# Kernel tuning notes

Hardware: AMD Instinct MI355X
Metric: run time of the kernel (lower is better)

Reference implementation:

```python
import jax, jax.numpy as jnp
import numpy as np

N_EMB = 1024
HEAD_SIZE = 128


def setup_inputs() -> dict:
    key = jax.random.key(0)
    k1, k2, k3, k4 = jax.random.split(key, 4)
    B, T = 8, 4096
    x = jax.random.normal(k1, (B, T, N_EMB), dtype=jnp.float32)
    # nn.Linear(n_emb, head_size, bias=False) weights have shape [head_size, n_emb]
    s = 1.0 / np.sqrt(N_EMB)
    Wq = jax.random.uniform(k2, (HEAD_SIZE, N_EMB), jnp.float32, -s, s)
    Wk = jax.random.uniform(k3, (HEAD_SIZE, N_EMB), jnp.float32, -s, s)
    Wv = jax.random.uniform(k4, (HEAD_SIZE, N_EMB), jnp.float32, -s, s)
    return {"x": x, "Wq": Wq, "Wk": Wk, "Wv": Wv}


def reference(x, Wq, Wk, Wv):
    # x: [B, T, C]; W*: [H, C]
    B, T, C = x.shape
    H = Wq.shape[0]
    q = jnp.einsum('btc,hc->bth', x, Wq)
    k = jnp.einsum('btc,hc->bth', x, Wk)
    v = jnp.einsum('btc,hc->bth', x, Wv)
    scale = H ** -0.5
    wei = jnp.einsum('bth,bsh->bts', q, k) * scale  # [B, T, T]
    # causal mask: position t attends to s <= t
    causal = jnp.arange(T)[:, None] >= jnp.arange(T)[None, :]
    wei = jnp.where(causal, wei, -jnp.inf)
    wei = jax.nn.softmax(wei, axis=-1)
    # dropout treated as identity (eval mode)
    out = jnp.einsum('bts,bsh->bth', wei, v)  # [B, T, H]
    return out
```

## Files before the change

kernel.cpp:

```cpp
#include <hip/hip_runtime.h>
#include <hip/hip_bf16.h>

typedef __bf16 bf16_t;
typedef __attribute__((ext_vector_type(8))) __bf16 bf16x8;
typedef __attribute__((ext_vector_type(4))) __bf16 bf16x4;
typedef __attribute__((ext_vector_type(4))) float f32x4;

#define MFMA16(a, b, c) __builtin_amdgcn_mfma_f32_16x16x32_bf16((a), (b), (c), 0, 0, 0)

__device__ __forceinline__ void gload_lds16(const void* g, void* l) {
    __builtin_amdgcn_global_load_lds(
        (const __attribute__((address_space(1))) void*)g,
        (__attribute__((address_space(3))) void*)l, 16, 0, 0);
}

__global__ __launch_bounds__(256, 3) void proj_qkv(
    const float* __restrict__ X,
    const float* __restrict__ W0, const float* __restrict__ W1, const float* __restrict__ W2,
    bf16_t* __restrict__ O0, bf16_t* __restrict__ O1, bf16_t* __restrict__ O2)
{
    __shared__ __align__(16) char As[128 * 128];
    __shared__ __align__(16) char Bs[128 * 128];

    const int tid = threadIdx.x;
    const int wid = tid >> 6;
    const int lane = tid & 63;
    const int l15 = lane & 15, l4 = lane >> 4;
    const int wr = wid >> 1, wc = wid & 1;
    const int m0 = blockIdx.x * 128;

    const float* W = (blockIdx.y == 0) ? W0 : (blockIdx.y == 1 ? W1 : W2);

    const int r0 = tid >> 4;
    const int kq = tid & 15;
    const int swz = ((r0 & 7) << 4);

    f32x4 acc[4][4] = {};
    float4 xr[8];

    #pragma unroll
    for (int i = 0; i < 8; ++i)
        xr[i] = *(const float4*)(X + (size_t)(m0 + r0 + i * 16) * 1024 + kq * 4);

    for (int ks = 0; ks < 16; ++ks) {
        const int kb = ks * 64;
        #pragma unroll
        for (int i = 0; i < 8; ++i) {
            const int r = r0 + i * 16;
            bf16x4 av; av[0] = (bf16_t)xr[i].x; av[1] = (bf16_t)xr[i].y;
            av[2] = (bf16_t)xr[i].z; av[3] = (bf16_t)xr[i].w;
            *(bf16x4*)(As + r * 128 + ((kq * 8) ^ swz)) = av;
        }
        #pragma unroll
        for (int i = 0; i < 8; ++i) {
            const int r = r0 + i * 16;
            float4 wa = *(const float4*)(W + (size_t)r * 1024 + kb + kq * 4);
            bf16x4 wv; wv[0] = (bf16_t)wa.x; wv[1] = (bf16_t)wa.y;
            wv[2] = (bf16_t)wa.z; wv[3] = (bf16_t)wa.w;
            *(bf16x4*)(Bs + r * 128 + ((kq * 8) ^ swz)) = wv;
        }
        __syncthreads();
        if (ks < 15) {
            #pragma unroll
            for (int i = 0; i < 8; ++i)
                xr[i] = *(const float4*)(X + (size_t)(m0 + r0 + i * 16) * 1024 + kb + 64 + kq * 4);
        }
        #pragma unroll
        for (int kk = 0; kk < 64; kk += 32) {
            const int kbyte = 2 * kk + 16 * l4;
            bf16x8 af[4], bfr[4];
            #pragma unroll
            for (int mi = 0; mi < 4; ++mi) {
                int r = wr * 64 + mi * 16 + l15;
                af[mi] = *(const bf16x8*)(As + r * 128 + (kbyte ^ ((r & 7) << 4)));
            }
            #pragma unroll
            for (int ni = 0; ni < 4; ++ni) {
                int r = wc * 64 + ni * 16 + l15;
                bfr[ni] = *(const bf16x8*)(Bs + r * 128 + (kbyte ^ ((r & 7) << 4)));
            }
            #pragma unroll
            for (int mi = 0; mi < 4; ++mi)
                #pragma unroll
                for (int ni = 0; ni < 4; ++ni)
                    acc[mi][ni] = MFMA16(af[mi], bfr[ni], acc[mi][ni]);
        }
        __syncthreads();
    }

    if (blockIdx.y < 2) {
        const float sc = (blockIdx.y == 0) ? 0.12751754816f : 1.0f;
        bf16_t* O = (blockIdx.y == 0) ? O0 : O1;
        #pragma unroll
        for (int mi = 0; mi < 4; ++mi)
            #pragma unroll
            for (int ni = 0; ni < 4; ++ni) {
                int row = m0 + wr * 64 + mi * 16 + l4 * 4;
                int col = wc * 64 + ni * 16 + l15;
                #pragma unroll
                for (int r = 0; r < 4; ++r)
                    O[(size_t)(row + r) * 128 + col] = (bf16_t)(acc[mi][ni][r] * sc);
            }
    } else {
        #pragma unroll
        for (int mi = 0; mi < 4; ++mi)
            #pragma unroll
            for (int ni = 0; ni < 4; ++ni) {
                int row0 = m0 + wr * 64 + mi * 16 + l4 * 4;
                int col = wc * 64 + ni * 16 + l15;
                int bb = row0 >> 12, t0 = row0 & 4095;
                bf16x4 pk;
                #pragma unroll
                for (int r = 0; r < 4; ++r) pk[r] = (bf16_t)acc[mi][ni][r];
                *(bf16x4*)(O2 + ((size_t)bb << 19) + (size_t)col * 4096 + t0) = pk;
            }
    }
}

__global__ __launch_bounds__(256, 2) void attn_fwd(
    const bf16_t* __restrict__ Qb, const bf16_t* __restrict__ Kb,
    const bf16_t* __restrict__ Vtg, float* __restrict__ out, int Bn)
{
    __shared__ __align__(16) char lds[73728];

    const int tid = threadIdx.x, wid = tid >> 6, lane = tid & 63;
    const int l15 = lane & 15, l4 = lane >> 4;
    const int pair = wid >> 1, qh = wid & 1;

    const int blk = blockIdx.x;
    const int b = blk % Bn;
    const int j = blk / Bn;

    const size_t base = (size_t)b * 4096 * 128;
    const size_t baseVT = (size_t)b << 19;

    char* Kbuf = lds + pair * 32768;
    char* Vbuf = Kbuf + 16384;
    char* Pw   = lds + 65536 + wid * 2048;
    const int key = l15 & 7;

    bf16x8 aones;
    #pragma unroll
    for (int e = 0; e < 8; ++e) aones[e] = (bf16_t)1.0f;

    for (int seg = 0; seg < 2; ++seg) {
        const int p = seg ? (127 - j) : j;
        const int q0 = p << 5;
        const int T = (p >> 1) + 1;
        const int smax = (T + 1) >> 1;
        const int qg = q0 + 16 * qh + l15;

        bf16x8 aq[4];
        #pragma unroll
        for (int kf = 0; kf < 4; ++kf)
            aq[kf] = *(const bf16x8*)(Qb + base + (size_t)qg * 128 + 32 * kf + 8 * l4);

        float mx = -1e30f;
        f32x4 ls_acc = (f32x4){0.f, 0.f, 0.f, 0.f};
        f32x4 o[8] = {};

        auto stage = [&](int s) {
            const int lt = 2 * s + pair;
            if (lt >= T) return;
            const int kv0 = lt << 6;
            if (qh == 0) {
                #pragma unroll
                for (int it = 0; it < 16; ++it) {
                    const int row = it * 4 + (lane >> 4);
                    const bf16_t* src = Kb + base + (size_t)(kv0 + row) * 128
                                        + (((lane & 15) ^ (row & 7)) << 3);
                    gload_lds16(src, Kbuf + it * 1024);
                }
            } else {
                #pragma unroll
                for (int it = 0; it < 16; ++it) {
                    const int h = it * 8 + (lane >> 3);
                    const bf16_t* src = Vtg + baseVT + (size_t)h * 4096 + kv0
                                        + (((lane & 7) ^ ((lane >> 3) & 7)) << 3);
                    gload_lds16(src, Vbuf + it * 1024);
                }
            }
        };

        __syncthreads();
        stage(0);
        __syncthreads();

        for (int s = 0; s < smax; ++s) {
            const int lt = 2 * s + pair;
            if (lt < T) {
                const int kv0 = lt << 6;

                f32x4 sa[4];
                #pragma unroll
                for (int ni = 0; ni < 4; ++ni) sa[ni] = (f32x4){0.f, 0.f, 0.f, 0.f};
                __builtin_amdgcn_s_setprio(1);
                #pragma unroll
                for (int kf = 0; kf < 4; ++kf)
                    #pragma unroll
                    for (int ni = 0; ni < 4; ++ni) {
                        bf16x8 ak = *(const bf16x8*)(Kbuf + (16 * ni + l15) * 256
                                                     + (((4 * kf + l4) ^ key) << 4));
                        sa[ni] = MFMA16(ak, aq[kf], sa[ni]);
                    }
                __builtin_amdgcn_s_setprio(0);

                if (lt == T - 1) {
                    #pragma unroll
                    for (int ni = 0; ni < 4; ++ni)
                        #pragma unroll
                        for (int r = 0; r < 4; ++r)
                            if (kv0 + 16 * ni + 4 * l4 + r > qg) sa[ni][r] = -1e30f;
                }

                float tm = -1e30f;
                #pragma unroll
                for (int ni = 0; ni < 4; ++ni)
                    tm = fmaxf(tm, fmaxf(fmaxf(sa[ni][0], sa[ni][1]),
                                         fmaxf(sa[ni][2], sa[ni][3])));
                if (__any(tm > mx + 8.0f)) {
                    tm = fmaxf(tm, __shfl_xor(tm, 16, 64));
                    tm = fmaxf(tm, __shfl_xor(tm, 32, 64));
                    const float mnew = fmaxf(mx, tm);
                    const float c = exp2f(mx - mnew);
                    ls_acc[0] *= c; ls_acc[1] *= c; ls_acc[2] *= c; ls_acc[3] *= c;
                    #pragma unroll
                    for (int mf = 0; mf < 8; ++mf) {
                        f32x4 t = o[mf];
                        t[0] *= c; t[1] *= c; t[2] *= c; t[3] *= c;
                        o[mf] = t;
                    }
                    mx = mnew;
                }
                #pragma unroll
                for (int ni = 0; ni < 4; ++ni) {
                    bf16x4 pv;
                    #pragma unroll
                    for (int r = 0; r < 4; ++r)
                        pv[r] = (bf16_t)exp2f(sa[ni][r] - mx);
                    *(bf16x4*)(Pw + l15 * 128
                               + (((2 * ni + (l4 >> 1)) ^ key) << 4) + 8 * (l4 & 1)) = pv;
                }

                __builtin_amdgcn_s_setprio(1);
                #pragma unroll
                for (int kfp = 0; kfp < 2; ++kfp) {
                    const int cb = ((4 * kfp + l4) ^ key) << 4;
                    bf16x8 pb = *(const bf16x8*)(Pw + l15 * 128 + cb);
                    ls_acc = MFMA16(aones, pb, ls_acc);
                    #pragma unroll
                    for (int mf = 0; mf < 8; ++mf) {
                        bf16x8 av = *(const bf16x8*)(Vbuf + (16 * mf + l15) * 128 + cb);
                        o[mf] = MFMA16(av, pb, o[mf]);
                    }
                }
                __builtin_amdgcn_s_setprio(0);
            }
            if (s + 1 < smax) {
                __syncthreads();
                stage(s + 1);
                __syncthreads();
            }
        }

        __syncthreads();
        if (pair == 1) {
            char* dst = lds + qh * 8192;
            #pragma unroll
            for (int mf = 0; mf < 8; ++mf)
                *(f32x4*)(dst + mf * 1024 + lane * 16) = o[mf];
            *(float2*)(lds + 49152 + qh * 512 + lane * 8) = make_float2(mx, ls_acc[0]);
        }
        __syncthreads();
        if (pair == 0) {
            float2 st = *(const float2*)(lds + 49152 + qh * 512 + lane * 8);
            const float mB = st.x, lB = st.y;
            const float M = fmaxf(mx, mB);
            const float a = exp2f(mx - M), b2 = exp2f(mB - M);
            const float linv = 1.f / (ls_acc[0] * a + lB * b2);
            char* srcO = lds + qh * 8192;
            float* op = out + ((size_t)b * 4096 + qg) * 128 + 4 * l4;
            #pragma unroll
            for (int mf = 0; mf < 8; ++mf) {
                f32x4 ob = *(const f32x4*)(srcO + mf * 1024 + lane * 16);
                f32x4 r;
                #pragma unroll
                for (int e = 0; e < 4; ++e) r[e] = (o[mf][e] * a + ob[e] * b2) * linv;
                *(f32x4*)(op + 16 * mf) = r;
            }
        }
    }
}

extern "C" void kernel_launch(void* const* d_in, const int* in_sizes, int n_in,
                              void* d_out, int out_size, void* d_ws, size_t ws_size,
                              hipStream_t stream) {
    const float* X  = (const float*)d_in[0];
    const float* Wq = (const float*)d_in[1];
    const float* Wk = (const float*)d_in[2];
    const float* Wv = (const float*)d_in[3];
    float* out = (float*)d_out;

    const int M = in_sizes[0] / 1024;
    const int Bn = M / 4096;

    bf16_t* Qb  = (bf16_t*)d_ws;
    bf16_t* KbP = Qb + (size_t)M * 128;
    bf16_t* VtP = KbP + (size_t)M * 128;

    proj_qkv<<<dim3(M / 128, 3), 256, 0, stream>>>(X, Wq, Wk, Wv, Qb, KbP, VtP);
    attn_fwd<<<dim3(64 * Bn), 256, 0, stream>>>(Qb, KbP, VtP, out, Bn);
}
```

Baseline: 125.6 us.

## Halve KV tile to 32 rows and double-buffer K/V loads in LDS

```diff
diff --git a/kernel.cpp b/kernel.cpp
--- a/kernel.cpp
+++ b/kernel.cpp
@@ -121,7 +121,7 @@
     const bf16_t* __restrict__ Qb, const bf16_t* __restrict__ Kb,
     const bf16_t* __restrict__ Vtg, float* __restrict__ out, int Bn)
 {
-    __shared__ __align__(16) char lds[73728];
+    __shared__ __align__(16) char lds[69632];
 
     const int tid = threadIdx.x, wid = tid >> 6, lane = tid & 63;
     const int l15 = lane & 15, l4 = lane >> 4;
@@ -134,10 +134,9 @@
     const size_t base = (size_t)b * 4096 * 128;
     const size_t baseVT = (size_t)b << 19;
 
-    char* Kbuf = lds + pair * 32768;
-    char* Vbuf = Kbuf + 16384;
-    char* Pw   = lds + 65536 + wid * 2048;
-    const int key = l15 & 7;
+    char* Pw = lds + 65536 + wid * 1024;
+    const int kkey = l15 & 7;
+    const int vkey = (l15 >> 1) & 3;
 
     bf16x8 aones;
     #pragma unroll
@@ -146,7 +145,7 @@
     for (int seg = 0; seg < 2; ++seg) {
         const int p = seg ? (127 - j) : j;
         const int q0 = p << 5;
-        const int T = (p >> 1) + 1;
+        const int T = p + 1;
         const int smax = (T + 1) >> 1;
         const int qg = q0 + 16 * qh + l15;
 
@@ -162,22 +161,24 @@
         auto stage = [&](int s) {
             const int lt = 2 * s + pair;
             if (lt >= T) return;
-            const int kv0 = lt << 6;
+            const int kv0 = lt << 5;
             if (qh == 0) {
-                #pragma unroll
-                for (int it = 0; it < 16; ++it) {
-                    const int row = it * 4 + (lane >> 4);
+                char* Kd = lds + pair * 16384 + (s & 1) * 8192;
+                #pragma unroll
+                for (int c = 0; c < 8; ++c) {
+                    const int row = c * 4 + (lane >> 4);
                     const bf16_t* src = Kb + base + (size_t)(kv0 + row) * 128
                                         + (((lane & 15) ^ (row & 7)) << 3);
-                    gload_lds16(src, Kbuf + it * 1024);
+                    gload_lds16(src, Kd + c * 1024);
                 }
             } else {
-                #pragma unroll
-                for (int it = 0; it < 16; ++it) {
-                    const int h = it * 8 + (lane >> 3);
-                    const bf16_t* src = Vtg + baseVT + (size_t)h * 4096 + kv0
-                                        + (((lane & 7) ^ ((lane >> 3) & 7)) << 3);
-                    gload_lds16(src, Vbuf + it * 1024);
+                char* Vd = lds + 32768 + pair * 16384 + (s & 1) * 8192;
+                #pragma unroll
+                for (int c = 0; c < 8; ++c) {
+                    const int row = c * 16 + (lane >> 2);
+                    const bf16_t* src = Vtg + baseVT + (size_t)row * 4096 + kv0
+                                        + (((lane & 3) ^ ((lane >> 3) & 3)) << 3);
+                    gload_lds16(src, Vd + c * 1024);
                 }
             }
         };
@@ -187,37 +188,39 @@
         __syncthreads();
 
         for (int s = 0; s < smax; ++s) {
+            if (s + 1 < smax) stage(s + 1);
             const int lt = 2 * s + pair;
             if (lt < T) {
-                const int kv0 = lt << 6;
-
-                f32x4 sa[4];
-                #pragma unroll
-                for (int ni = 0; ni < 4; ++ni) sa[ni] = (f32x4){0.f, 0.f, 0.f, 0.f};
+                const int kv0 = lt << 5;
+                char* Kbuf = lds + pair * 16384 + (s & 1) * 8192;
+                char* Vbuf = lds + 32768 + pair * 16384 + (s & 1) * 8192;
+
+                f32x4 sa[2];
+                #pragma unroll
+                for (int ni = 0; ni < 2; ++ni) sa[ni] = (f32x4){0.f, 0.f, 0.f, 0.f};
                 __builtin_amdgcn_s_setprio(1);
                 #pragma unroll
                 for (int kf = 0; kf < 4; ++kf)
                     #pragma unroll
-                    for (int ni = 0; ni < 4; ++ni) {
+                    for (int ni = 0; ni < 2; ++ni) {
                         bf16x8 ak = *(const bf16x8*)(Kbuf + (16 * ni + l15) * 256
-                                                     + (((4 * kf + l4) ^ key) << 4));
+                                                     + (((4 * kf + l4) ^ kkey) << 4));
                         sa[ni] = MFMA16(ak, aq[kf], sa[ni]);
                     }
                 __builtin_amdgcn_s_setprio(0);
 
                 if (lt == T - 1) {
                     #pragma unroll
-                    for (int ni = 0; ni < 4; ++ni)
+                    for (int ni = 0; ni < 2; ++ni)
                         #pragma unroll
                         for (int r = 0; r < 4; ++r)
                             if (kv0 + 16 * ni + 4 * l4 + r > qg) sa[ni][r] = -1e30f;
                 }
 
-                float tm = -1e30f;
-                #pragma unroll
-                for (int ni = 0; ni < 4; ++ni)
-                    tm = fmaxf(tm, fmaxf(fmaxf(sa[ni][0], sa[ni][1]),
-                                         fmaxf(sa[ni][2], sa[ni][3])));
+                float tm = fmaxf(fmaxf(fmaxf(sa[0][0], sa[0][1]),
+                                       fmaxf(sa[0][2], sa[0][3])),
+                                 fmaxf(fmaxf(sa[1][0], sa[1][1]),
+                                       fmaxf(sa[1][2], sa[1][3])));
                 if (__any(tm > mx + 8.0f)) {
                     tm = fmaxf(tm, __shfl_xor(tm, 16, 64));
                     tm = fmaxf(tm, __shfl_xor(tm, 32, 64));
@@ -233,34 +236,27 @@
                     mx = mnew;
                 }
                 #pragma unroll
-                for (int ni = 0; ni < 4; ++ni) {
+                for (int ni = 0; ni < 2; ++ni) {
                     bf16x4 pv;
                     #pragma unroll
                     for (int r = 0; r < 4; ++r)
                         pv[r] = (bf16_t)exp2f(sa[ni][r] - mx);
-                    *(bf16x4*)(Pw + l15 * 128
-                               + (((2 * ni + (l4 >> 1)) ^ key) << 4) + 8 * (l4 & 1)) = pv;
-                }
-
+                    *(bf16x4*)(Pw + l15 * 64
+                               + (((2 * ni + (l4 >> 1)) ^ vkey) << 4) + 8 * (l4 & 1)) = pv;
+                }
+
+                bf16x8 pb = *(const bf16x8*)(Pw + l15 * 64 + ((l4 ^ vkey) << 4));
                 __builtin_amdgcn_s_setprio(1);
-                #pragma unroll
-                for (int kfp = 0; kfp < 2; ++kfp) {
-                    const int cb = ((4 * kfp + l4) ^ key) << 4;
-                    bf16x8 pb = *(const bf16x8*)(Pw + l15 * 128 + cb);
-                    ls_acc = MFMA16(aones, pb, ls_acc);
-                    #pragma unroll
-                    for (int mf = 0; mf < 8; ++mf) {
-                        bf16x8 av = *(const bf16x8*)(Vbuf + (16 * mf + l15) * 128 + cb);
-                        o[mf] = MFMA16(av, pb, o[mf]);
-                    }
+                ls_acc = MFMA16(aones, pb, ls_acc);
+                #pragma unroll
+                for (int mf = 0; mf < 8; ++mf) {
+                    bf16x8 av = *(const bf16x8*)(Vbuf + (16 * mf + l15) * 64
+                                                 + ((l4 ^ vkey) << 4));
+                    o[mf] = MFMA16(av, pb, o[mf]);
                 }
                 __builtin_amdgcn_s_setprio(0);
             }
-            if (s + 1 < smax) {
-                __syncthreads();
-                stage(s + 1);
-                __syncthreads();
-            }
+            __syncthreads();
         }
 
         __syncthreads();
```

New measurement: 128.3 us. +2.2%, slower.
